# Optimization experiments

Hardware: AMD Instinct MI355X
Metric: run time of the kernel (lower is better)

The kernel has to match this reference:

```python
import jax, jax.numpy as jnp
import numpy as np

H = 256; DS = 8; DC = 4; DI = 512; DTR = 16; NH = 4; EPS = 1e-5
B, N, F, E, S, LC = 8, 512, 32, 8192, 512, 8


def setup_inputs() -> dict:
    key = jax.random.key(0)
    ks = iter(jax.random.split(key, 64))
    def rn(shape, s=0.05):
        return jax.random.normal(next(ks), shape, jnp.float32) * s
    z = lambda *s: jnp.zeros(s, jnp.float32)
    inp = dict(
        node_features=jax.random.normal(next(ks), (B, N, F), jnp.float32),
        edge_index=jax.random.randint(next(ks), (B, 2, E), 0, N),
        W_init=rn((F, H)), b_init=z(H),
        gcn1_W=rn((H, H)), gcn1_b=z(H),
        gcn2_W=rn((H, H)), gcn2_b=z(H),
        in_proj_W=rn((H, 2 * DI)),
        conv_W=rn((DI, DC)), conv_b=z(DI),
        xproj_W=rn((DI, DTR + 2 * DS)),
        dt_W=rn((DTR, DI)), dt_b=z(DI),
        A_log=jnp.log(jnp.tile(jnp.arange(1, DS + 1, dtype=jnp.float32), (DI, 1))),
        Dp=jnp.ones((DI,), jnp.float32),
        out_W=rn((DI, H)),
        Wq=rn((H, H)), bq=z(H), Wk=rn((H, H)), bk=z(H), Wv=rn((H, H)), bv=z(H),
        Wo=rn((H, H)), bo=z(H),
        fus_W=rn((3 * H, H)), fus_b=z(H),
        ln_g=jnp.ones((H,), jnp.float32), ln_b=z(H),
        cw=rn((H, 1)), cb=z(1), hw=rn((H, 4)), hb=z(4), tw=rn((H, 3)), tb=z(3),
        p1w=rn((H, S)), p1b=z(S), p2w=rn((H, S)), p2b=z(S),
        dw=rn((H, S)), db=z(S), sw=rn((H, LC)), sb=z(LC))
    return inp


def gcn(x, src, dst, W, b):
    # PyG GCNConv: self-loops + symmetric deg^{-1/2} normalization, scatter-add.
    n = x.shape[0]
    loops = jnp.arange(n)
    s = jnp.concatenate([src, loops]); d = jnp.concatenate([dst, loops])
    deg = jax.ops.segment_sum(jnp.ones_like(d, x.dtype), d, n)
    dinv = jnp.where(deg > 0, jax.lax.rsqrt(deg), 0.0)
    norm = (dinv[s] * dinv[d])[:, None]
    m = x @ W
    return jax.ops.segment_sum(m[s] * norm, d, n) + b


def mamba(x, in_W, conv_W, conv_b, xproj_W, dt_W, dt_b, A_log, Dp, out_W):
    # mamba_ssm Mamba block, batch=1, seq len L = total nodes.
    L = x.shape[0]
    xz = x @ in_W
    xc, zg = xz[:, :DI], xz[:, DI:]
    xp = jnp.pad(xc, ((DC - 1, 0), (0, 0)))            # causal depthwise conv
    win = xp[jnp.arange(L)[:, None] + jnp.arange(DC)[None, :]]  # [L,K,DI]
    xc = jax.nn.silu(jnp.einsum('lkd,dk->ld', win, conv_W) + conv_b)
    proj = xc @ xproj_W
    dt, Bm, Cm = proj[:, :DTR], proj[:, DTR:DTR + DS], proj[:, DTR + DS:]
    delta = jax.nn.softplus(dt @ dt_W + dt_b)           # [L,DI]
    A = -jnp.exp(A_log)                                 # [DI,DS]
    dA = jnp.exp(delta[:, :, None] * A[None])           # [L,DI,DS]
    dBx = delta[:, :, None] * Bm[:, None, :] * xc[:, :, None]
    def step(h, inp):
        dA_t, dBx_t, C_t = inp
        h = dA_t * h + dBx_t
        return h, (h * C_t[None, :]).sum(-1)
    _, y = jax.lax.scan(step, jnp.zeros((DI, DS), x.dtype), (dA, dBx, Cm))
    y = (y + Dp * xc) * jax.nn.silu(zg)
    return y @ out_W


def mha(x, Wq, bq, Wk, bk, Wv, bv, Wo, bo):
    L = x.shape[0]; hd = H // NH
    q = (x @ Wq + bq).reshape(L, NH, hd)
    k = (x @ Wk + bk).reshape(L, NH, hd)
    v = (x @ Wv + bv).reshape(L, NH, hd)
    s = jnp.einsum('qhd,khd->hqk', q, k) / np.float32(np.sqrt(hd))
    a = jax.nn.softmax(s, axis=-1)
    o = jnp.einsum('hqk,khd->qhd', a, v).reshape(L, H)
    return o @ Wo + bo


def _forward(node_features, edge_index, W_init, b_init, gcn1_W, gcn1_b, gcn2_W, gcn2_b,
             in_proj_W, conv_W, conv_b, xproj_W, dt_W, dt_b, A_log, Dp, out_W,
             Wq, bq, Wk, bk, Wv, bv, Wo, bo, fus_W, fus_b, ln_g, ln_b,
             cw, cb, hw, hb, tw, tb, p1w, p1b, p2w, p2b, dw, db, sw, sb):
    Bsz, Nn, Ff = node_features.shape
    x = node_features.reshape(Bsz * Nn, Ff)
    # offset per-graph edge indices into the flat node space (batching loop)
    ei = (edge_index + (jnp.arange(Bsz) * Nn)[:, None, None]).transpose(1, 0, 2).reshape(2, -1)
    src, dst = ei[0], ei[1]
    h = jax.nn.relu(x @ W_init + b_init)
    h = jax.nn.relu(gcn(h, src, dst, gcn1_W, gcn1_b))
    h = jax.nn.relu(gcn(h, src, dst, gcn2_W, gcn2_b))
    m = mamba(h, in_proj_W, conv_W, conv_b, xproj_W, dt_W, dt_b, A_log, Dp, out_W)
    a = mha(h, Wq, bq, Wk, bk, Wv, bv, Wo, bo)
    fused = jax.nn.relu(jnp.concatenate([h, m, a], -1) @ fus_W + fus_b)
    res = fused + h
    mu = res.mean(-1, keepdims=True)
    var = ((res - mu) ** 2).mean(-1, keepdims=True)
    hf = (res - mu) * jax.lax.rsqrt(var + EPS) * ln_g + ln_b
    batch = jnp.repeat(jnp.arange(Bsz), Nn)
    pooled = jax.ops.segment_sum(hf, batch, Bsz) / jnp.float32(Nn)  # global_mean_pool
    outs = [pooled @ cw + cb, pooled @ hw + hb, pooled @ tw + tb,
            pooled @ p1w + p1b, pooled @ p2w + p2b, pooled @ dw + db,
            pooled @ sw + sb]
    return jnp.concatenate(outs, -1)  # [B, 1+4+3+S+S+S+LC]


def reference(node_features, edge_index, W_init, b_init, gcn1_W, gcn1_b, gcn2_W, gcn2_b,
              in_proj_W, conv_W, conv_b, xproj_W, dt_W, dt_b, A_log, Dp, out_W,
              Wq, bq, Wk, bk, Wv, bv, Wo, bo, fus_W, fus_b, ln_g, ln_b,
              cw, cb, hw, hb, tw, tb, p1w, p1b, p2w, p2b, dw, db, sw, sb):
    return _forward(node_features, edge_index, W_init, b_init, gcn1_W, gcn1_b, gcn2_W, gcn2_b,
                    in_proj_W, conv_W, conv_b, xproj_W, dt_W, dt_b, A_log, Dp, out_W,
                    Wq, bq, Wk, bk, Wv, bv, Wo, bo, fus_W, fus_b, ln_g, ln_b,
                    cw, cb, hw, hb, tw, tb, p1w, p1b, p2w, p2b, dw, db, sw, sb)
```

## Files before the change

kernel.cpp:

```cpp
#include <hip/hip_runtime.h>
#include <hip/hip_bf16.h>
#include <math.h>

typedef __hip_bfloat16 hbf;
typedef short bf16x8 __attribute__((ext_vector_type(8)));
typedef float f32x4 __attribute__((ext_vector_type(4)));

constexpr int NL  = 4096;
constexpr int HH  = 256;
constexpr int NE  = 8192;
constexpr int DIc = 512;
constexpr int DSc = 8;
constexpr int CLc = 16;
constexpr int NOUT = 12416;

constexpr size_t O_MBUF  = 0;
constexpr size_t O_QK    = 1048576;
constexpr size_t O_H2    = 2097152;
constexpr size_t O_CATB  = 3145728;
constexpr size_t O_XZB   = 4718592;
constexpr size_t O_XC    = 6815744;
constexpr size_t O_DELTA = 8912896;
constexpr size_t O_PROJ  = 11010048;
constexpr size_t O_HST   = 11141120;
constexpr size_t O_Y     = 12189696;
constexpr size_t O_POOL  = 13238272;
constexpr size_t O_DINV  = 13240320;
constexpr size_t O_B768  = 13244416;
constexpr size_t O_INT   = 13245184;
constexpr size_t O_WT    = 13327112;
constexpr size_t O_XB    = 13839112;
constexpr size_t O_H0B   = 13904648;
constexpr size_t O_H2B   = 14428936;
constexpr size_t O_XCB   = 14953224;
constexpr size_t O_DTAB  = 16001800;
constexpr size_t O_QKB   = 16067584;
constexpr size_t O_VTB   = 17116160;
constexpr size_t O_PART  = 17640448;

constexpr int NW = 12;
__device__ __constant__ int wc_cum[NW+1] = {
    0, 8192, 73728, 139264, 155648, 172032, 303104, 565248,
    630784, 696320, 761856, 827392, 1024000 };
__device__ __constant__ int wc_K [NW] = {32,256,256,512,16,512,256,256,256,256,256,768};
__device__ __constant__ int wc_N [NW] = {256,256,256,32,512,256,1024,256,256,256,256,256};
__device__ __constant__ int wc_Kp[NW] = {32,256,256,512,32,512,256,256,256,256,256,768};
struct WSrc { const float* p[NW]; };
struct OPtrs { hbf* p[8]; };

constexpr int PR_W = 1024000;
constexpr int PR_X = PR_W + 131072;
constexpr int PR_B = PR_X + 768;
constexpr int PR_P = PR_B + 262144;
constexpr int PR_I = PR_P + 4096;
__global__ __launch_bounds__(256) void prep_k(WSrc ws, hbf* __restrict__ wt,
        const float* __restrict__ x, hbf* __restrict__ xb,
        const float* __restrict__ bq, const float* __restrict__ bk,
        const float* __restrict__ bv,
        float* __restrict__ b768, float* __restrict__ part, int* __restrict__ indeg) {
    int idx = blockIdx.x*256 + threadIdx.x;
    if (idx < PR_W) {
        int lo = 0, hi = NW-1;
        while (lo < hi) { int mid = (lo+hi+1)>>1; if (idx >= wc_cum[mid]) lo = mid; else hi = mid-1; }
        int local = idx - wc_cum[lo];
        int Kp = wc_Kp[lo], K = wc_K[lo], N = wc_N[lo];
        int n = local / Kp, k = local - n*Kp;
        float v = (k < K) ? ws.p[lo][(size_t)k*N + n] : 0.0f;
        wt[idx] = __float2bfloat16(v);
    } else if (idx < PR_X) {
        int i = idx - PR_W;
        xb[i] = __float2bfloat16(x[i]);
    } else if (idx < PR_B) {
        int i = idx - PR_X;
        b768[i] = (i < 256) ? bq[i] : (i < 512 ? bk[i-256] : bv[i-512]);
    } else if (idx < PR_P) {
        part[idx - PR_B] = 0.0f;
    } else if (idx < PR_I) {
        indeg[idx - PR_P] = 0;
    }
}

__global__ void count_k(const int* __restrict__ ei, int* __restrict__ indeg) {
    int i = blockIdx.x*256 + threadIdx.x;
    int b = i >> 13, e = i & 8191;
    int dst = ei[b*2*NE + NE + e] + (b << 9);
    atomicAdd(&indeg[dst], 1);
}

__global__ __launch_bounds__(1024) void prefix_k(const int* __restrict__ indeg,
                                                 int* __restrict__ row_start,
                                                 int* __restrict__ cursor,
                                                 float* __restrict__ dinv) {
    __shared__ int part[1024];
    int t = threadIdx.x;
    int v0[4]; int s = 0;
    #pragma unroll
    for (int i = 0; i < 4; i++) {
        int cnt = indeg[t*4 + i];
        v0[i] = s; s += cnt;
        dinv[t*4 + i] = rsqrtf(1.0f + (float)cnt);
    }
    part[t] = s;
    __syncthreads();
    for (int o = 1; o < 1024; o <<= 1) {
        int x = (t >= o) ? part[t-o] : 0;
        __syncthreads();
        part[t] += x;
        __syncthreads();
    }
    int base = (t > 0) ? part[t-1] : 0;
    #pragma unroll
    for (int i = 0; i < 4; i++) {
        int rs = base + v0[i];
        row_start[t*4+i] = rs; cursor[t*4+i] = rs;
    }
    if (t == 1023) row_start[4096] = part[1023];
}

__global__ void scatter_k(const int* __restrict__ ei, int* __restrict__ cursor,
                          int* __restrict__ csr) {
    int i = blockIdx.x*256 + threadIdx.x;
    int b = i >> 13, e = i & 8191;
    int src = ei[b*2*NE + e]       + (b << 9);
    int dst = ei[b*2*NE + NE + e]  + (b << 9);
    int pos = atomicAdd(&cursor[dst], 1);
    csr[pos] = src;
}

template<int MODE>
__global__ __launch_bounds__(256) void gather_k(const float* __restrict__ m,
                        const int* __restrict__ csr, const int* __restrict__ row_start,
                        const float* __restrict__ dinv, const float* __restrict__ bias,
                        float* __restrict__ out, hbf* __restrict__ outb,
                        hbf* __restrict__ catb) {
    int n = blockIdx.x, c = threadIdx.x;
    float dn = dinv[n];
    float acc = m[(size_t)n*HH + c] * dn * dn;
    int e0 = row_start[n], e1 = row_start[n+1];
    for (int e = e0; e < e1; e++) {
        int s = csr[e];
        acc += m[(size_t)s*HH + c] * (dinv[s] * dn);
    }
    float r = fmaxf(acc + bias[c], 0.0f);
    if (MODE) {
        out[(size_t)n*HH + c] = r;
        catb[(size_t)n*768 + c] = __float2bfloat16(r);
    }
    outb[(size_t)n*HH + c] = __float2bfloat16(r);
}

template<int ACT, int OUTM>
__global__ __launch_bounds__(512) void mg_k(const unsigned short* __restrict__ A,
        const unsigned short* __restrict__ Bt, const float* __restrict__ bias,
        void* __restrict__ Cp, int ldc, void* __restrict__ Cp2, void* __restrict__ Cp3,
        const float* __restrict__ resid, int ldr, int M, int K, int N)
{
    __shared__ __align__(16) unsigned short Asm[2][64][40];
    __shared__ __align__(16) unsigned short Bsm[2][64][40];
    int t = threadIdx.x;
    int lane = t & 63, w = t >> 6;
    int wm = w & 3, wn = w >> 2;
    int row0 = blockIdx.x * 64, col0 = blockIdx.y * 64;
    int sr = t >> 3;
    int sk8 = (t & 7) * 8;
    int su = sk8 >> 5, so = sk8 & 31;
    f32x4 acc0 = {}, acc1 = {};
    int fr = lane & 15, fq8 = (lane >> 4) * 8;

    uint4 zz = make_uint4(0u,0u,0u,0u);
    uint4 ra = zz, rb = zz;
    bool bnv = (col0 + sr) < N;
    if (sk8 < K) {
        ra = *(const uint4*)&A[(size_t)(row0+sr)*K + sk8];
        if (bnv) rb = *(const uint4*)&Bt[(size_t)(col0+sr)*K + sk8];
    }

    for (int k0 = 0; k0 < K; k0 += 64) {
        __syncthreads();
        *(uint4*)&Asm[su][sr][so] = ra;
        *(uint4*)&Bsm[su][sr][so] = rb;
        __syncthreads();
        int kn = k0 + 64;
        if (kn < K) {
            ra = rb = zz;
            if (kn + sk8 < K) {
                ra = *(const uint4*)&A[(size_t)(row0+sr)*K + kn + sk8];
                if (bnv) rb = *(const uint4*)&Bt[(size_t)(col0+sr)*K + kn + sk8];
            }
        }
        #pragma unroll
        for (int ks = 0; ks < 2; ks++) {
            bf16x8 a  = *(bf16x8*)&Asm[ks][wm*16 + fr][fq8];
            bf16x8 b0 = *(bf16x8*)&Bsm[ks][wn*32 + fr][fq8];
            bf16x8 b1 = *(bf16x8*)&Bsm[ks][wn*32 + 16 + fr][fq8];
            acc0 = __builtin_amdgcn_mfma_f32_16x16x32_bf16(a, b0, acc0, 0, 0, 0);
            acc1 = __builtin_amdgcn_mfma_f32_16x16x32_bf16(a, b1, acc1, 0, 0, 0);
        }
    }

    int fc = lane & 15, frq = (lane >> 4) * 4;
    if constexpr (OUTM == 4) {
        #pragma unroll
        for (int nt = 0; nt < 2; nt++) {
            int col = col0 + wn*32 + nt*16 + fc;
            if (col >= 32) continue;
            f32x4& av = nt ? acc1 : acc0;
            #pragma unroll
            for (int i = 0; i < 4; i++) {
                int row = row0 + wm*16 + frq + i;
                float v = av[i];
                ((float*)Cp)[(size_t)row*32 + col] = v;
                ((hbf*)Cp2)[(size_t)row*32 + col] = __float2bfloat16((col < 16) ? v : 0.0f);
            }
        }
    } else if constexpr (OUTM == 5) {
        if (col0 < 1024) {
            #pragma unroll
            for (int nt = 0; nt < 2; nt++) {
                int col = col0 + wn*32 + nt*16 + fc;
                f32x4& av = nt ? acc1 : acc0;
                #pragma unroll
                for (int i = 0; i < 4; i++) {
                    int row = row0 + wm*16 + frq + i;
                    ((hbf*)Cp)[(size_t)row*1024 + col] = __float2bfloat16(av[i]);
                }
            }
        } else if (col0 < 1536) {
            #pragma unroll
            for (int nt = 0; nt < 2; nt++) {
                int gcol = col0 + wn*32 + nt*16 + fc;
                int col = gcol - 1024;
                float bvv = bias[col];
                float sc = (col < 256) ? 0.125f : 1.0f;
                f32x4& av = nt ? acc1 : acc0;
                #pragma unroll
                for (int i = 0; i < 4; i++) {
                    int row = row0 + wm*16 + frq + i;
                    ((hbf*)Cp2)[(size_t)row*512 + col] = __float2bfloat16((av[i] + bvv) * sc);
                }
            }
        } else {
            __shared__ __align__(16) unsigned short Ts[64][72];
            #pragma unroll
            for (int nt = 0; nt < 2; nt++) {
                int gcol = col0 + wn*32 + nt*16 + fc;
                float bvv = bias[gcol - 1024];
                f32x4& av = nt ? acc1 : acc0;
                #pragma unroll
                for (int i = 0; i < 4; i++)
                    *(hbf*)&Ts[wn*32 + nt*16 + fc][wm*16 + frq + i] = __float2bfloat16(av[i] + bvv);
            }
            __syncthreads();
            int c = t >> 3, rs = (t & 7) * 8;
            *(uint4*)((hbf*)Cp3 + (size_t)(col0 - 1536 + c)*NL + row0 + rs) = *(uint4*)&Ts[c][rs];
        }
    } else {
        #pragma unroll
        for (int nt = 0; nt < 2; nt++) {
            int col = col0 + wn*32 + nt*16 + fc;
            if (col >= N) continue;
            float bvv = bias ? bias[col] : 0.0f;
            f32x4& av = nt ? acc1 : acc0;
            #pragma unroll
            for (int i = 0; i < 4; i++) {
                int row = row0 + wm*16 + frq + i;
                float v = av[i] + bvv;
                if (ACT == 1) v = fmaxf(v, 0.0f);
                if (ACT == 2) v = (v > 20.0f) ? v : log1pf(expf(v));
                if (resid) v += resid[(size_t)row*ldr + col];
                if (OUTM == 0) ((float*)Cp)[(size_t)row*ldc + col] = v;
                else           ((hbf*)Cp)[(size_t)row*ldc + col] = __float2bfloat16(v);
            }
        }
    }
}

__global__ void conv_k(const hbf* __restrict__ xzb, const float* __restrict__ cW,
                       const float* __restrict__ cb, float* __restrict__ xc2,
                       hbf* __restrict__ xcb) {
    int i = blockIdx.x*256 + threadIdx.x;
    int l = i >> 9, d = i & 511;
    float acc = cb[d];
    #pragma unroll
    for (int k = 0; k < 4; k++) {
        int ls = l - 3 + k;
        if (ls >= 0) acc += __bfloat162float(xzb[(size_t)ls*1024 + d]) * cW[d*4 + k];
    }
    float r = acc / (1.0f + __expf(-acc));
    xc2[i] = r;
    xcb[i] = __float2bfloat16(r);
}

__global__ __launch_bounds__(256) void scan1_k(const float* __restrict__ delta,
                        const float* __restrict__ xc, const float* __restrict__ proj,
                        const float* __restrict__ Alog,
                        float* __restrict__ P, float* __restrict__ Hl)
{
    int c = blockIdx.x >> 1;
    int d = ((blockIdx.x & 1) << 8) + threadIdx.x;
    float Ac[DSc], pr[DSc], h[DSc];
    #pragma unroll
    for (int s2 = 0; s2 < DSc; s2++) { Ac[s2] = -__expf(Alog[d*DSc+s2]); pr[s2]=1.0f; h[s2]=0.0f; }
    int l0 = c * CLc;
    for (int l = l0; l < l0 + CLc; l++) {
        float dl = delta[(size_t)l*DIc + d];
        float dx = dl * xc[(size_t)l*DIc + d];
        const float* pb = proj + l*32 + 16;
        #pragma unroll
        for (int s2 = 0; s2 < DSc; s2++) {
            float a = __expf(dl * Ac[s2]);
            h[s2] = a*h[s2] + dx*pb[s2];
            pr[s2] *= a;
        }
    }
    #pragma unroll
    for (int s2 = 0; s2 < DSc; s2++) {
        P [(size_t)(c*DSc+s2)*DIc + d] = pr[s2];
        Hl[(size_t)(c*DSc+s2)*DIc + d] = h[s2];
    }
}

__global__ __launch_bounds__(256) void scan2p_k(const float* __restrict__ P,
                        const float* __restrict__ Hl, float* __restrict__ Hst) {
    __shared__ float Psh[256], Hsh[256];
    int t = threadIdx.x, series = blockIdx.x;
    size_t off = (size_t)t*4096 + series;
    float Pc = P[off], Hc = Hl[off];
    Psh[t] = Pc; Hsh[t] = Hc;
    __syncthreads();
    #pragma unroll
    for (int st = 1; st < 256; st <<= 1) {
        float p1 = 1.0f, h1 = 0.0f;
        if (t >= st) { p1 = Psh[t-st]; h1 = Hsh[t-st]; }
        __syncthreads();
        Hc = Pc*h1 + Hc;
        Pc = Pc*p1;
        Psh[t] = Pc; Hsh[t] = Hc;
        __syncthreads();
    }
    Hst[off] = (t == 0) ? 0.0f : Hsh[t-1];
}

__global__ __launch_bounds__(256) void scan3_k(const float* __restrict__ delta,
                        const float* __restrict__ xc, const float* __restrict__ proj,
                        const float* __restrict__ Alog, const float* __restrict__ Hst,
                        const float* __restrict__ Dp, const hbf* __restrict__ xzb,
                        hbf* __restrict__ Y)
{
    int c = blockIdx.x >> 1;
    int d = ((blockIdx.x & 1) << 8) + threadIdx.x;
    float Ac[DSc], h[DSc];
    #pragma unroll
    for (int s2 = 0; s2 < DSc; s2++) {
        Ac[s2] = -__expf(Alog[d*DSc+s2]);
        h[s2]  = Hst[(size_t)(c*DSc+s2)*DIc + d];
    }
    float dpv = Dp[d];
    int l0 = c * CLc;
    for (int l = l0; l < l0 + CLc; l++) {
        float dl = delta[(size_t)l*DIc + d];
        float xv = xc[(size_t)l*DIc + d];
        float dx = dl * xv;
        const float* pb = proj + l*32 + 16;
        float y = 0.0f;
        #pragma unroll
        for (int s2 = 0; s2 < DSc; s2++) {
            float a = __expf(dl * Ac[s2]);
            h[s2] = a*h[s2] + dx*pb[s2];
            y += h[s2] * pb[8+s2];
        }
        float z = __bfloat162float(xzb[(size_t)l*1024 + 512 + d]);
        float sz = z / (1.0f + __expf(-z));
        Y[(size_t)l*DIc + d] = __float2bfloat16((y + dpv*xv) * sz);
    }
}

__global__ __launch_bounds__(256) void attn_part_k(const unsigned short* __restrict__ QK,
                       const unsigned short* __restrict__ Vt,
                       OPtrs op, float* __restrict__ lsum)
{
    __shared__ __align__(16) unsigned short QPs[128][72];
    __shared__ __align__(16) unsigned short Ks[64][72];
    __shared__ __align__(16) unsigned short Vs[64][72];
    int t = threadIdx.x, lane = t & 63, w = t >> 6;
    int h = blockIdx.y, q0 = blockIdx.x * 128, skc = blockIdx.z;
    int fm = lane & 15, fq = lane >> 4;

    {
        int qr = t >> 1, qc = (t & 1) * 32;
        const unsigned short* src = &QK[(size_t)(q0+qr)*512 + h*64 + qc];
        *(uint4*)&QPs[qr][qc]      = *(const uint4*)&src[0];
        *(uint4*)&QPs[qr][qc + 8]  = *(const uint4*)&src[8];
        *(uint4*)&QPs[qr][qc + 16] = *(const uint4*)&src[16];
        *(uint4*)&QPs[qr][qc + 24] = *(const uint4*)&src[24];
    }
    __syncthreads();
    bf16x8 qa[2][2];
    #pragma unroll
    for (int rf = 0; rf < 2; rf++)
        #pragma unroll
        for (int ks = 0; ks < 2; ks++)
            qa[rf][ks] = *(bf16x8*)&QPs[w*32 + rf*16 + fm][ks*32 + fq*8];

    bf16x8 ones;
    #pragma unroll
    for (int j = 0; j < 8; j++) ones[j] = (short)0x3F80;

    f32x4 o[2][4] = {};
    f32x4 ol[2] = {};
    int sr = t >> 2, sk = (t & 3) * 16;
    const unsigned short* Kb = QK + 256;
    int kt = skc * 512;
    uint4 ka  = *(const uint4*)&Kb[(size_t)(kt+sr)*512 + h*64 + sk];
    uint4 kb2 = *(const uint4*)&Kb[(size_t)(kt+sr)*512 + h*64 + sk + 8];
    uint4 va  = *(const uint4*)&Vt[(size_t)(h*64+sr)*NL + kt + sk];
    uint4 vb2 = *(const uint4*)&Vt[(size_t)(h*64+sr)*NL + kt + sk + 8];

    for (int it = 0; it < 8; it++) {
        __syncthreads();
        *(uint4*)&Ks[sr][sk] = ka;  *(uint4*)&Ks[sr][sk+8] = kb2;
        *(uint4*)&Vs[sr][sk] = va;  *(uint4*)&Vs[sr][sk+8] = vb2;
        __syncthreads();
        if (it < 7) {
            int kn = kt + 64;
            ka  = *(const uint4*)&Kb[(size_t)(kn+sr)*512 + h*64 + sk];
            kb2 = *(const uint4*)&Kb[(size_t)(kn+sr)*512 + h*64 + sk + 8];
            va  = *(const uint4*)&Vt[(size_t)(h*64+sr)*NL + kn + sk];
            vb2 = *(const uint4*)&Vt[(size_t)(h*64+sr)*NL + kn + sk + 8];
        }
        f32x4 s[2][4] = {};
        #pragma unroll
        for (int ks = 0; ks < 2; ks++) {
            #pragma unroll
            for (int nt = 0; nt < 4; nt++) {
                bf16x8 kb = *(bf16x8*)&Ks[nt*16 + fm][ks*32 + fq*8];
                s[0][nt] = __builtin_amdgcn_mfma_f32_16x16x32_bf16(qa[0][ks], kb, s[0][nt], 0, 0, 0);
                s[1][nt] = __builtin_amdgcn_mfma_f32_16x16x32_bf16(qa[1][ks], kb, s[1][nt], 0, 0, 0);
            }
        }
        #pragma unroll
        for (int rf = 0; rf < 2; rf++)
            #pragma unroll
            for (int nt = 0; nt < 4; nt++)
                #pragma unroll
                for (int i = 0; i < 4; i++) {
                    float p = __expf(s[rf][nt][i] - 4.0f);
                    *(hbf*)&QPs[w*32 + rf*16 + fq*4 + i][nt*16 + fm] = __float2bfloat16(p);
                }
        #pragma unroll
        for (int ks = 0; ks < 2; ks++) {
            bf16x8 pa0 = *(bf16x8*)&QPs[w*32 + fm][ks*32 + fq*8];
            bf16x8 pa1 = *(bf16x8*)&QPs[w*32 + 16 + fm][ks*32 + fq*8];
            #pragma unroll
            for (int nt = 0; nt < 4; nt++) {
                bf16x8 vb = *(bf16x8*)&Vs[nt*16 + fm][ks*32 + fq*8];
                o[0][nt] = __builtin_amdgcn_mfma_f32_16x16x32_bf16(pa0, vb, o[0][nt], 0, 0, 0);
                o[1][nt] = __builtin_amdgcn_mfma_f32_16x16x32_bf16(pa1, vb, o[1][nt], 0, 0, 0);
            }
            ol[0] = __builtin_amdgcn_mfma_f32_16x16x32_bf16(pa0, ones, ol[0], 0, 0, 0);
            ol[1] = __builtin_amdgcn_mfma_f32_16x16x32_bf16(pa1, ones, ol[1], 0, 0, 0);
        }
        kt += 64;
    }
    hbf* Op = op.p[skc];
    #pragma unroll
    for (int rf = 0; rf < 2; rf++)
        #pragma unroll
        for (int i = 0; i < 4; i++) {
            int row = w*32 + rf*16 + fq*4 + i;
            #pragma unroll
            for (int nt = 0; nt < 4; nt++)
                Op[(size_t)(q0 + row)*HH + h*64 + nt*16 + fm] = __float2bfloat16(o[rf][nt][i]);
        }
    if (fm == 0) {
        #pragma unroll
        for (int rf = 0; rf < 2; rf++)
            #pragma unroll
            for (int i = 0; i < 4; i++)
                lsum[(size_t)(skc*4 + h)*NL + q0 + w*32 + rf*16 + fq*4 + i] = ol[rf][i];
    }
}

__global__ __launch_bounds__(256) void amerge_k(OPtrs op, const float* __restrict__ lsum,
                                                hbf* __restrict__ aob) {
    int row = blockIdx.x, t = threadIdx.x, h = t >> 6;
    float L = 0.0f, s = 0.0f;
    #pragma unroll
    for (int c = 0; c < 8; c++) {
        L += lsum[(size_t)(c*4 + h)*NL + row];
        s += __bfloat162float(op.p[c][(size_t)row*HH + t]);
    }
    aob[(size_t)row*HH + t] = __float2bfloat16(s / L);
}

__global__ __launch_bounds__(256) void ln_k(const float* __restrict__ X,
                    const float* __restrict__ g, const float* __restrict__ b,
                    float* __restrict__ part) {
    __shared__ float red[4];
    int r = blockIdx.x, t = threadIdx.x;
    float v = X[(size_t)r*HH + t];
    float s = v;
    #pragma unroll
    for (int o = 32; o > 0; o >>= 1) s += __shfl_down(s, o);
    if ((t & 63) == 0) red[t >> 6] = s;
    __syncthreads();
    float mean = (red[0]+red[1]+red[2]+red[3]) * (1.0f/256.0f);
    float dfv = v - mean;
    float s2 = dfv*dfv;
    #pragma unroll
    for (int o = 32; o > 0; o >>= 1) s2 += __shfl_down(s2, o);
    __syncthreads();
    if ((t & 63) == 0) red[t >> 6] = s2;
    __syncthreads();
    float var = (red[0]+red[1]+red[2]+red[3]) * (1.0f/256.0f);
    float y = dfv * rsqrtf(var + 1e-5f) * g[t] + b[t];
    atomicAdd(&part[(size_t)(r & 127)*2048 + (r >> 9)*HH + t], y * (1.0f/512.0f));
}

__global__ void reduce_k(const float* __restrict__ part, float* __restrict__ pooled) {
    int i = blockIdx.x*256 + threadIdx.x;
    float s = 0.0f;
    #pragma unroll 8
    for (int p = 0; p < 128; p++) s += part[(size_t)p*2048 + i];
    pooled[i] = s;
}

__global__ __launch_bounds__(256) void heads_k(const float* __restrict__ pooled,
        const float* cw, const float* cbh, const float* hw, const float* hb,
        const float* tw, const float* tb, const float* p1w, const float* p1b,
        const float* p2w, const float* p2b, const float* dw, const float* db,
        const float* sw, const float* sb, float* __restrict__ out)
{
    int idx = blockIdx.x*4 + (threadIdx.x >> 6);
    int lane = threadIdx.x & 63;
    if (idx >= NOUT) return;
    int b = idx / 1552, j = idx - b*1552;
    const float* w; const float* bi; int col, nc;
    if (j < 1)         { w = cw;  bi = cbh; col = j;        nc = 1;   }
    else if (j < 5)    { w = hw;  bi = hb;  col = j - 1;    nc = 4;   }
    else if (j < 8)    { w = tw;  bi = tb;  col = j - 5;    nc = 3;   }
    else if (j < 520)  { w = p1w; bi = p1b; col = j - 8;    nc = 512; }
    else if (j < 1032) { w = p2w; bi = p2b; col = j - 520;  nc = 512; }
    else if (j < 1544) { w = dw;  bi = db;  col = j - 1032; nc = 512; }
    else               { w = sw;  bi = sb;  col = j - 1544; nc = 8;   }
    const float* pl = pooled + b*HH;
    float s = 0.0f;
    #pragma unroll
    for (int k = lane; k < 256; k += 64) s = fmaf(pl[k], w[(size_t)k*nc + col], s);
    #pragma unroll
    for (int o = 32; o > 0; o >>= 1) s += __shfl_down(s, o);
    if (lane == 0) out[idx] = s + bi[col];
}

extern "C" void kernel_launch(void* const* d_in, const int* in_sizes, int n_in,
                              void* d_out, int out_size, void* d_ws, size_t ws_size,
                              hipStream_t stream)
{
    (void)in_sizes; (void)n_in; (void)out_size; (void)ws_size;
    const float* x      = (const float*)d_in[0];
    const int*   ei     = (const int*)  d_in[1];
    const float* W_init = (const float*)d_in[2];
    const float* b_init = (const float*)d_in[3];
    const float* g1W = (const float*)d_in[4];
    const float* g1b = (const float*)d_in[5];
    const float* g2W = (const float*)d_in[6];
    const float* g2b = (const float*)d_in[7];
    const float* inW = (const float*)d_in[8];
    const float* cW  = (const float*)d_in[9];
    const float* cb  = (const float*)d_in[10];
    const float* xpW = (const float*)d_in[11];
    const float* dtW = (const float*)d_in[12];
    const float* dtb = (const float*)d_in[13];
    const float* Alog= (const float*)d_in[14];
    const float* Dp  = (const float*)d_in[15];
    const float* outW= (const float*)d_in[16];
    const float* Wq  = (const float*)d_in[17];
    const float* bq  = (const float*)d_in[18];
    const float* Wk  = (const float*)d_in[19];
    const float* bk  = (const float*)d_in[20];
    const float* Wv  = (const float*)d_in[21];
    const float* bv  = (const float*)d_in[22];
    const float* Wo  = (const float*)d_in[23];
    const float* bo  = (const float*)d_in[24];
    const float* fusW= (const float*)d_in[25];
    const float* fusb= (const float*)d_in[26];
    const float* lng = (const float*)d_in[27];
    const float* lnb = (const float*)d_in[28];
    const float* cwp = (const float*)d_in[29];
    const float* cbp = (const float*)d_in[30];
    const float* hwp = (const float*)d_in[31];
    const float* hbp = (const float*)d_in[32];
    const float* twp = (const float*)d_in[33];
    const float* tbp = (const float*)d_in[34];
    const float* p1w = (const float*)d_in[35];
    const float* p1b = (const float*)d_in[36];
    const float* p2w = (const float*)d_in[37];
    const float* p2b = (const float*)d_in[38];
    const float* dwp = (const float*)d_in[39];
    const float* dbp = (const float*)d_in[40];
    const float* swp = (const float*)d_in[41];
    const float* sbp = (const float*)d_in[42];

    float* fw = (float*)d_ws;
    int* iw = (int*)(fw + O_INT);
    int* indeg = iw;
    int* row_start = iw + 4096;
    int* cursor = iw + 8193;
    int* csr = iw + 12289;
    float* dinv = fw + O_DINV;

    hbf* wt   = (hbf*)(fw + O_WT);
    hbf* xb   = (hbf*)(fw + O_XB);
    hbf* h0b  = (hbf*)(fw + O_H0B);
    hbf* h2b  = (hbf*)(fw + O_H2B);
    hbf* xcb  = (hbf*)(fw + O_XCB);
    hbf* dtab = (hbf*)(fw + O_DTAB);
    hbf* xzb  = (hbf*)(fw + O_XZB);
    hbf* yb   = (hbf*)(fw + O_Y);
    hbf* aob  = (hbf*)(fw + O_Y);
    hbf* catb = (hbf*)(fw + O_CATB);
    hbf* qkB  = (hbf*)(fw + O_QKB);
    hbf* vtB  = (hbf*)(fw + O_VTB);
    float* fused = fw + O_XC;
    float* b768 = fw + O_B768;
    float* part = fw + O_PART;

    float* scanP  = fw + O_MBUF;
    float* scanHl = fw + O_QK;
    float* scanHst= fw + O_HST;
    float* lsum   = fw + O_HST;

    OPtrs op;
    op.p[0] = (hbf*)(fw + O_MBUF);
    op.p[1] = (hbf*)(fw + O_MBUF + 524288);
    op.p[2] = (hbf*)(fw + O_DELTA);
    op.p[3] = (hbf*)(fw + O_DELTA + 524288);
    op.p[4] = (hbf*)(fw + O_DELTA + 1048576);
    op.p[5] = (hbf*)(fw + O_DELTA + 1572864);
    op.p[6] = (hbf*)(fw + O_XZB);
    op.p[7] = (hbf*)(fw + O_XZB + 524288);

    hbf* WtInit  = wt + 0;
    hbf* WtG1    = wt + 8192;
    hbf* WtG2    = wt + 73728;
    hbf* WtXp    = wt + 139264;
    hbf* WtDt    = wt + 155648;
    hbf* WtOut   = wt + 172032;
    hbf* WtInQKV = wt + 303104;
    hbf* WtO     = wt + 761856;
    hbf* WtFus   = wt + 827392;

    WSrc wsrc;
    wsrc.p[0]=W_init; wsrc.p[1]=g1W; wsrc.p[2]=g2W; wsrc.p[3]=xpW; wsrc.p[4]=dtW;
    wsrc.p[5]=outW; wsrc.p[6]=inW; wsrc.p[7]=Wq; wsrc.p[8]=Wk; wsrc.p[9]=Wv;
    wsrc.p[10]=Wo; wsrc.p[11]=fusW;
    prep_k<<<(PR_I+255)/256,256,0,stream>>>(wsrc, wt, x, xb, bq, bk, bv, b768,
                                            part, indeg);

    count_k<<<256,256,0,stream>>>(ei, indeg);
    prefix_k<<<1,1024,0,stream>>>(indeg, row_start, cursor, dinv);
    scatter_k<<<256,256,0,stream>>>(ei, cursor, csr);

    mg_k<1,1><<<dim3(64,4),512,0,stream>>>((const unsigned short*)xb, (const unsigned short*)WtInit,
        b_init, h0b, 256, nullptr, nullptr, nullptr, 0, NL, 32, 256);
    mg_k<0,0><<<dim3(64,4),512,0,stream>>>((const unsigned short*)h0b, (const unsigned short*)WtG1,
        nullptr, fw+O_MBUF, 256, nullptr, nullptr, nullptr, 0, NL, 256, 256);
    gather_k<0><<<4096,256,0,stream>>>(fw+O_MBUF, csr, row_start, dinv, g1b, nullptr, h0b, nullptr);
    mg_k<0,0><<<dim3(64,4),512,0,stream>>>((const unsigned short*)h0b, (const unsigned short*)WtG2,
        nullptr, fw+O_MBUF, 256, nullptr, nullptr, nullptr, 0, NL, 256, 256);
    gather_k<1><<<4096,256,0,stream>>>(fw+O_MBUF, csr, row_start, dinv, g2b, fw+O_H2, h2b, catb);

    mg_k<0,5><<<dim3(64,28),512,0,stream>>>((const unsigned short*)h2b, (const unsigned short*)WtInQKV,
        b768, xzb, 1024, qkB, vtB, nullptr, 0, NL, 256, 1792);

    conv_k<<<8192,256,0,stream>>>(xzb, cW, cb, fw+O_XC, xcb);
    mg_k<0,4><<<dim3(64,1),512,0,stream>>>((const unsigned short*)xcb, (const unsigned short*)WtXp,
        nullptr, fw+O_PROJ, 32, dtab, nullptr, nullptr, 0, NL, 512, 32);
    mg_k<2,0><<<dim3(64,8),512,0,stream>>>((const unsigned short*)dtab, (const unsigned short*)WtDt,
        dtb, fw+O_DELTA, 512, nullptr, nullptr, nullptr, 0, NL, 32, 512);
    scan1_k<<<512,256,0,stream>>>(fw+O_DELTA, fw+O_XC, fw+O_PROJ, Alog, scanP, scanHl);
    scan2p_k<<<4096,256,0,stream>>>(scanP, scanHl, scanHst);
    scan3_k<<<512,256,0,stream>>>(fw+O_DELTA, fw+O_XC, fw+O_PROJ, Alog, scanHst, Dp, xzb, yb);
    mg_k<0,1><<<dim3(64,4),512,0,stream>>>((const unsigned short*)yb, (const unsigned short*)WtOut,
        nullptr, catb + 256, 768, nullptr, nullptr, nullptr, 0, NL, 512, 256);

    attn_part_k<<<dim3(32,4,8),256,0,stream>>>((const unsigned short*)qkB,
        (const unsigned short*)vtB, op, lsum);
    amerge_k<<<4096,256,0,stream>>>(op, lsum, aob);
    mg_k<0,1><<<dim3(64,4),512,0,stream>>>((const unsigned short*)aob, (const unsigned short*)WtO,
        bo, catb + 512, 768, nullptr, nullptr, nullptr, 0, NL, 256, 256);

    mg_k<1,0><<<dim3(64,4),512,0,stream>>>((const unsigned short*)catb, (const unsigned short*)WtFus,
        fusb, fused, 256, nullptr, nullptr, fw+O_H2, 256, NL, 768, 256);
    ln_k<<<4096,256,0,stream>>>(fused, lng, lnb, part);
    reduce_k<<<8,256,0,stream>>>(part, fw+O_POOL);
    heads_k<<<(NOUT+3)/4,256,0,stream>>>(fw+O_POOL, cwp,cbp,hwp,hbp,twp,tbp,p1w,p1b,p2w,p2b,
                                         dwp,dbp,swp,sbp, (float*)d_out);
}
```

Before: 374.1 us.

## Restructure chunk-state scan, drop fp32 conv output, pre-transpose head weights

The middle pass of the chunked selective scan is rewritten so each block handles 16 series through shared memory. Each thread does a serial 16-chunk pass, then a 16-lane shuffle scan, instead of a 256-step Hillis-Steele scan with many barriers per series. The fp32 copy of the conv output is dropped and the scan kernels read the bf16 copy, which cuts memory traffic but lowers precision for the scan input. Head weights are transposed once in the prep kernel so that heads_k reads contiguous rows rather than strided columns, at the cost of extra prep work.

After: 352.6 us. -5.8%, faster.

```diff
diff --git a/kernel.cpp b/kernel.cpp
--- a/kernel.cpp
+++ b/kernel.cpp
@@ -37,6 +37,7 @@
 constexpr size_t O_QKB   = 16067584;
 constexpr size_t O_VTB   = 17116160;
 constexpr size_t O_PART  = 17640448;
+constexpr size_t O_HWT   = 17902592;
 
 constexpr int NW = 12;
 __device__ __constant__ int wc_cum[NW+1] = {
@@ -46,18 +47,24 @@
 __device__ __constant__ int wc_N [NW] = {256,256,256,32,512,256,1024,256,256,256,256,256};
 __device__ __constant__ int wc_Kp[NW] = {32,256,256,512,32,512,256,256,256,256,256,768};
 struct WSrc { const float* p[NW]; };
+struct HSrc { const float* p[7]; };
 struct OPtrs { hbf* p[8]; };
+
+__device__ __constant__ int hw_b[8]  = {0,1,5,8,520,1032,1544,1552};
+__device__ __constant__ int hw_nc[7] = {1,4,3,512,512,512,8};
 
 constexpr int PR_W = 1024000;
 constexpr int PR_X = PR_W + 131072;
 constexpr int PR_B = PR_X + 768;
 constexpr int PR_P = PR_B + 262144;
 constexpr int PR_I = PR_P + 4096;
+constexpr int PR_H = PR_I + 397312;
 __global__ __launch_bounds__(256) void prep_k(WSrc ws, hbf* __restrict__ wt,
         const float* __restrict__ x, hbf* __restrict__ xb,
         const float* __restrict__ bq, const float* __restrict__ bk,
         const float* __restrict__ bv,
-        float* __restrict__ b768, float* __restrict__ part, int* __restrict__ indeg) {
+        float* __restrict__ b768, float* __restrict__ part, int* __restrict__ indeg,
+        HSrc hs, float* __restrict__ hwt) {
     int idx = blockIdx.x*256 + threadIdx.x;
     if (idx < PR_W) {
         int lo = 0, hi = NW-1;
@@ -77,6 +84,13 @@
         part[idx - PR_B] = 0.0f;
     } else if (idx < PR_I) {
         indeg[idx - PR_P] = 0;
+    } else if (idx < PR_H) {
+        int i = idx - PR_I;
+        int j = i >> 8, k = i & 255;
+        int seg = 0;
+        while (j >= hw_b[seg+1]) seg++;
+        int col = j - hw_b[seg], nc = hw_nc[seg];
+        hwt[(size_t)j*256 + k] = hs.p[seg][(size_t)k*nc + col];
     }
 }
 
@@ -276,8 +290,7 @@
 }
 
 __global__ void conv_k(const hbf* __restrict__ xzb, const float* __restrict__ cW,
-                       const float* __restrict__ cb, float* __restrict__ xc2,
-                       hbf* __restrict__ xcb) {
+                       const float* __restrict__ cb, hbf* __restrict__ xcb) {
     int i = blockIdx.x*256 + threadIdx.x;
     int l = i >> 9, d = i & 511;
     float acc = cb[d];
@@ -287,12 +300,11 @@
         if (ls >= 0) acc += __bfloat162float(xzb[(size_t)ls*1024 + d]) * cW[d*4 + k];
     }
     float r = acc / (1.0f + __expf(-acc));
-    xc2[i] = r;
     xcb[i] = __float2bfloat16(r);
 }
 
 __global__ __launch_bounds__(256) void scan1_k(const float* __restrict__ delta,
-                        const float* __restrict__ xc, const float* __restrict__ proj,
+                        const hbf* __restrict__ xc, const float* __restrict__ proj,
                         const float* __restrict__ Alog,
                         float* __restrict__ P, float* __restrict__ Hl)
 {
@@ -304,7 +316,7 @@
     int l0 = c * CLc;
     for (int l = l0; l < l0 + CLc; l++) {
         float dl = delta[(size_t)l*DIc + d];
-        float dx = dl * xc[(size_t)l*DIc + d];
+        float dx = dl * __bfloat162float(xc[(size_t)l*DIc + d]);
         const float* pb = proj + l*32 + 16;
         #pragma unroll
         for (int s2 = 0; s2 < DSc; s2++) {
@@ -320,29 +332,55 @@
     }
 }
 
-__global__ __launch_bounds__(256) void scan2p_k(const float* __restrict__ P,
+__global__ __launch_bounds__(256) void scan2t_k(const float* __restrict__ P,
                         const float* __restrict__ Hl, float* __restrict__ Hst) {
-    __shared__ float Psh[256], Hsh[256];
-    int t = threadIdx.x, series = blockIdx.x;
-    size_t off = (size_t)t*4096 + series;
-    float Pc = P[off], Hc = Hl[off];
-    Psh[t] = Pc; Hsh[t] = Hc;
+    __shared__ float Ps[256][17], Hs[256][17];
+    int t = threadIdx.x, sg = blockIdx.x;
+    int si = t & 15, cb = t >> 4;
+    #pragma unroll
+    for (int it = 0; it < 16; it++) {
+        int c = it*16 + cb;
+        size_t off = (size_t)c*4096 + sg*16 + si;
+        Ps[c][si] = P[off];
+        Hs[c][si] = Hl[off];
+    }
     __syncthreads();
-    #pragma unroll
-    for (int st = 1; st < 256; st <<= 1) {
-        float p1 = 1.0f, h1 = 0.0f;
-        if (t >= st) { p1 = Psh[t-st]; h1 = Hsh[t-st]; }
-        __syncthreads();
-        Hc = Pc*h1 + Hc;
-        Pc = Pc*p1;
-        Psh[t] = Pc; Hsh[t] = Hc;
-        __syncthreads();
-    }
-    Hst[off] = (t == 0) ? 0.0f : Hsh[t-1];
+    int si2 = t >> 4, g = t & 15;
+    int lane = t & 63;
+    float Pg = 1.0f, Hg = 0.0f;
+    #pragma unroll
+    for (int j = 0; j < 16; j++) {
+        int c = g*16 + j;
+        float pc = Ps[c][si2], hc = Hs[c][si2];
+        Hg = hc + pc*Hg;
+        Pg = pc*Pg;
+    }
+    #pragma unroll
+    for (int off = 1; off < 16; off <<= 1) {
+        float Pp = __shfl(Pg, lane - off);
+        float Hp = __shfl(Hg, lane - off);
+        if (g >= off) { Hg = Hg + Pg*Hp; Pg = Pg*Pp; }
+    }
+    float carry = __shfl(Hg, lane - 1);
+    if (g == 0) carry = 0.0f;
+    float h = carry;
+    #pragma unroll
+    for (int j = 0; j < 16; j++) {
+        int c = g*16 + j;
+        float pc = Ps[c][si2], hc = Hs[c][si2];
+        Hs[c][si2] = h;
+        h = hc + pc*h;
+    }
+    __syncthreads();
+    #pragma unroll
+    for (int it = 0; it < 16; it++) {
+        int c = it*16 + cb;
+        Hst[(size_t)c*4096 + sg*16 + si] = Hs[c][si];
+    }
 }
 
 __global__ __launch_bounds__(256) void scan3_k(const float* __restrict__ delta,
-                        const float* __restrict__ xc, const float* __restrict__ proj,
+                        const hbf* __restrict__ xc, const float* __restrict__ proj,
                         const float* __restrict__ Alog, const float* __restrict__ Hst,
                         const float* __restrict__ Dp, const hbf* __restrict__ xzb,
                         hbf* __restrict__ Y)
@@ -359,7 +397,7 @@
     int l0 = c * CLc;
     for (int l = l0; l < l0 + CLc; l++) {
         float dl = delta[(size_t)l*DIc + d];
-        float xv = xc[(size_t)l*DIc + d];
+        float xv = __bfloat162float(xc[(size_t)l*DIc + d]);
         float dx = dl * xv;
         const float* pb = proj + l*32 + 16;
         float y = 0.0f;
@@ -526,27 +564,27 @@
 }
 
 __global__ __launch_bounds__(256) void heads_k(const float* __restrict__ pooled,
-        const float* cw, const float* cbh, const float* hw, const float* hb,
-        const float* tw, const float* tb, const float* p1w, const float* p1b,
-        const float* p2w, const float* p2b, const float* dw, const float* db,
-        const float* sw, const float* sb, float* __restrict__ out)
+        const float* __restrict__ hwt,
+        const float* cbh, const float* hb, const float* tb, const float* p1b,
+        const float* p2b, const float* db, const float* sb, float* __restrict__ out)
 {
     int idx = blockIdx.x*4 + (threadIdx.x >> 6);
     int lane = threadIdx.x & 63;
     if (idx >= NOUT) return;
     int b = idx / 1552, j = idx - b*1552;
-    const float* w; const float* bi; int col, nc;
-    if (j < 1)         { w = cw;  bi = cbh; col = j;        nc = 1;   }
-    else if (j < 5)    { w = hw;  bi = hb;  col = j - 1;    nc = 4;   }
-    else if (j < 8)    { w = tw;  bi = tb;  col = j - 5;    nc = 3;   }
-    else if (j < 520)  { w = p1w; bi = p1b; col = j - 8;    nc = 512; }
-    else if (j < 1032) { w = p2w; bi = p2b; col = j - 520;  nc = 512; }
-    else if (j < 1544) { w = dw;  bi = db;  col = j - 1032; nc = 512; }
-    else               { w = sw;  bi = sb;  col = j - 1544; nc = 8;   }
+    const float* bi; int col;
+    if (j < 1)         { bi = cbh; col = j;        }
+    else if (j < 5)    { bi = hb;  col = j - 1;    }
+    else if (j < 8)    { bi = tb;  col = j - 5;    }
+    else if (j < 520)  { bi = p1b; col = j - 8;    }
+    else if (j < 1032) { bi = p2b; col = j - 520;  }
+    else if (j < 1544) { bi = db;  col = j - 1032; }
+    else               { bi = sb;  col = j - 1544; }
     const float* pl = pooled + b*HH;
+    const float* wr = hwt + (size_t)j*256;
     float s = 0.0f;
     #pragma unroll
-    for (int k = lane; k < 256; k += 64) s = fmaf(pl[k], w[(size_t)k*nc + col], s);
+    for (int k = lane; k < 256; k += 64) s = fmaf(pl[k], wr[k], s);
     #pragma unroll
     for (int o = 32; o > 0; o >>= 1) s += __shfl_down(s, o);
     if (lane == 0) out[idx] = s + bi[col];
@@ -624,6 +662,7 @@
     float* fused = fw + O_XC;
     float* b768 = fw + O_B768;
     float* part = fw + O_PART;
+    float* hwt  = fw + O_HWT;
 
     float* scanP  = fw + O_MBUF;
     float* scanHl = fw + O_QK;
@@ -654,8 +693,11 @@
     wsrc.p[0]=W_init; wsrc.p[1]=g1W; wsrc.p[2]=g2W; wsrc.p[3]=xpW; wsrc.p[4]=dtW;
     wsrc.p[5]=outW; wsrc.p[6]=inW; wsrc.p[7]=Wq; wsrc.p[8]=Wk; wsrc.p[9]=Wv;
     wsrc.p[10]=Wo; wsrc.p[11]=fusW;
-    prep_k<<<(PR_I+255)/256,256,0,stream>>>(wsrc, wt, x, xb, bq, bk, bv, b768,
-                                            part, indeg);
+    HSrc hsrc;
+    hsrc.p[0]=cwp; hsrc.p[1]=hwp; hsrc.p[2]=twp; hsrc.p[3]=p1w;
+    hsrc.p[4]=p2w; hsrc.p[5]=dwp; hsrc.p[6]=swp;
+    prep_k<<<(PR_H+255)/256,256,0,stream>>>(wsrc, wt, x, xb, bq, bk, bv, b768,
+                                            part, indeg, hsrc, hwt);
 
     count_k<<<256,256,0,stream>>>(ei, indeg);
     prefix_k<<<1,1024,0,stream>>>(indeg, row_start, cursor, dinv);
@@ -673,14 +715,14 @@
     mg_k<0,5><<<dim3(64,28),512,0,stream>>>((const unsigned short*)h2b, (const unsigned short*)WtInQKV,
         b768, xzb, 1024, qkB, vtB, nullptr, 0, NL, 256, 1792);
 
-    conv_k<<<8192,256,0,stream>>>(xzb, cW, cb, fw+O_XC, xcb);
+    conv_k<<<8192,256,0,stream>>>(xzb, cW, cb, xcb);
     mg_k<0,4><<<dim3(64,1),512,0,stream>>>((const unsigned short*)xcb, (const unsigned short*)WtXp,
         nullptr, fw+O_PROJ, 32, dtab, nullptr, nullptr, 0, NL, 512, 32);
     mg_k<2,0><<<dim3(64,8),512,0,stream>>>((const unsigned short*)dtab, (const unsigned short*)WtDt,
         dtb, fw+O_DELTA, 512, nullptr, nullptr, nullptr, 0, NL, 32, 512);
-    scan1_k<<<512,256,0,stream>>>(fw+O_DELTA, fw+O_XC, fw+O_PROJ, Alog, scanP, scanHl);
-    scan2p_k<<<4096,256,0,stream>>>(scanP, scanHl, scanHst);
-    scan3_k<<<512,256,0,stream>>>(fw+O_DELTA, fw+O_XC, fw+O_PROJ, Alog, scanHst, Dp, xzb, yb);
+    scan1_k<<<512,256,0,stream>>>(fw+O_DELTA, xcb, fw+O_PROJ, Alog, scanP, scanHl);
+    scan2t_k<<<256,256,0,stream>>>(scanP, scanHl, scanHst);
+    scan3_k<<<512,256,0,stream>>>(fw+O_DELTA, xcb, fw+O_PROJ, Alog, scanHst, Dp, xzb, yb);
     mg_k<0,1><<<dim3(64,4),512,0,stream>>>((const unsigned short*)yb, (const unsigned short*)WtOut,
         nullptr, catb + 256, 768, nullptr, nullptr, nullptr, 0, NL, 512, 256);
 
@@ -694,6 +736,6 @@
         fusb, fused, 256, nullptr, nullptr, fw+O_H2, 256, NL, 768, 256);
     ln_k<<<4096,256,0,stream>>>(fused, lng, lnb, part);
     reduce_k<<<8,256,0,stream>>>(part, fw+O_POOL);
-    heads_k<<<(NOUT+3)/4,256,0,stream>>>(fw+O_POOL, cwp,cbp,hwp,hbp,twp,tbp,p1w,p1b,p2w,p2b,
-                                         dwp,dbp,swp,sbp, (float*)d_out);
-}
+    heads_k<<<(NOUT+3)/4,256,0,stream>>>(fw+O_POOL, hwt, cbp,hbp,tbp,p1b,p2b,dbp,sbp,
+                                         (float*)d_out);
+}
```
